# Kernel optimization log

Hardware: AMD Instinct MI355X
Metric: run time of the kernel (lower is better)

Reference implementation:

```python
import jax, jax.numpy as jnp
import numpy as np

N_NODES = 20000


def _gcn_conv(x, edge_index, W, b):
    """PyG GCNConv: add self-loops, symmetric normalization, x @ W, scatter-add, + bias."""
    n = x.shape[0]
    loops = jnp.arange(n, dtype=edge_index.dtype)
    src = jnp.concatenate([edge_index[0], loops])  # [E+N]
    dst = jnp.concatenate([edge_index[1], loops])  # [E+N]
    # degree of target nodes (edge weight 1), self-loops guarantee deg >= 1
    deg = jax.ops.segment_sum(jnp.ones_like(dst, dtype=x.dtype), dst, num_segments=n)
    dinv = jax.lax.rsqrt(deg)
    norm = dinv[src] * dinv[dst]  # [E+N]
    h = x @ W  # [n, out] dense GEMM before aggregation (standard GCNConv ordering)
    msg = h[src] * norm[:, None]  # gather + scale over edges
    out = jax.ops.segment_sum(msg, dst, num_segments=n)  # scatter-add to targets
    return out + b


def setup_inputs() -> dict:
    key = jax.random.key(0)
    k = jax.random.split(key, 6)
    in_f, h_f, n_cls = 512, 512, 256
    x = jax.random.normal(k[0], (N_NODES, in_f), dtype=jnp.float32)
    edge_index = jax.random.randint(k[1], (2, 160000), 0, N_NODES, dtype=jnp.int64)
    W1 = jax.random.normal(k[2], (in_f, h_f), dtype=jnp.float32) * (1.0 / np.sqrt(in_f))
    b1 = jnp.zeros((h_f,), dtype=jnp.float32)
    W2 = jax.random.normal(k[3], (h_f, n_cls), dtype=jnp.float32) * (1.0 / np.sqrt(h_f))
    b2 = jnp.zeros((n_cls,), dtype=jnp.float32)
    return {"x": x, "edge_index": edge_index, "W1": W1, "b1": b1, "W2": W2, "b2": b2}


def reference(x, edge_index, W1, b1, W2, b2):
    h = jax.nn.relu(_gcn_conv(x, edge_index, W1, b1))
    h = jax.nn.relu(_gcn_conv(h, edge_index, W2, b2))
    # F.dropout in eval mode is identity; reference is deterministic eval-mode forward
    return h
```

## Files before the change

kernel.cpp:

```cpp
#include <hip/hip_runtime.h>


typedef __bf16 bf16x8 __attribute__((ext_vector_type(8)));
typedef float floatx4 __attribute__((ext_vector_type(4)));
typedef unsigned short ushort_t;
typedef unsigned int uint_t;

#define MAXD 32
#define CAP 40

__device__ inline ushort_t f2bf(float f) {
    unsigned u = __builtin_bit_cast(unsigned, f);
    unsigned r = (u + 0x7FFFu + ((u >> 16) & 1u)) >> 16;
    return (ushort_t)r;
}
__device__ inline float bf_lo(uint_t u) { return __builtin_bit_cast(float, u << 16); }
__device__ inline float bf_hi(uint_t u) { return __builtin_bit_cast(float, u & 0xFFFF0000u); }
__device__ inline uint_t pk2(float lo, float hi) {
    return (uint_t)f2bf(lo) | ((uint_t)f2bf(hi) << 16);
}

__device__ inline void transpose_tile(const float* __restrict__ in,
                                      ushort_t* __restrict__ out,
                                      int K, int N, int k0, int n0,
                                      ushort_t (*tile)[33]) {
    int tx = threadIdx.x & 31, ty = threadIdx.x >> 5;
    for (int r = ty; r < 32; r += 8)
        tile[r][tx] = f2bf(in[(size_t)(k0 + r) * N + n0 + tx]);
    __syncthreads();
    for (int r = ty; r < 32; r += 8)
        out[(size_t)(n0 + r) * K + k0 + tx] = tile[tx][r];
}

__global__ __launch_bounds__(256) void prep_fused(
    const int* __restrict__ src, const int* __restrict__ dst,
    int* __restrict__ deg, int* __restrict__ col_ell,
    int* __restrict__ ovf_cnt, int* __restrict__ ovf, int e, int nb_e,
    const float* __restrict__ x, ushort_t* __restrict__ xb, long xcount, int nb_conv,
    const float* __restrict__ W1, ushort_t* __restrict__ w1t,
    const float* __restrict__ W2, ushort_t* __restrict__ w2t) {
    __shared__ ushort_t tile[32][33];
    int b = blockIdx.x;
    if (b < nb_e) {
        int i = b * 256 + threadIdx.x;
        if (i < e) {
            int s = src[i], d = dst[i];
            int slot = atomicAdd(&deg[d], 1);
            if (slot < MAXD) {
                col_ell[d * MAXD + slot] = s;
            } else {
                int k = atomicAdd(ovf_cnt, 1);
                ovf[2 * k] = d;
                ovf[2 * k + 1] = s;
            }
        }
        return;
    }
    b -= nb_e;
    if (b < nb_conv) {
        long i = ((long)b * 256 + threadIdx.x) * 4;
        if (i < xcount) {
            float4 v = *(const float4*)(x + i);
            ushort4 o = make_ushort4(f2bf(v.x), f2bf(v.y), f2bf(v.z), f2bf(v.w));
            *(ushort4*)(xb + i) = o;
        }
        return;
    }
    b -= nb_conv;
    if (b < 256) {
        transpose_tile(W1, w1t, 512, 512, (b >> 4) * 32, (b & 15) * 32, tile);
        return;
    }
    b -= 256;
    transpose_tile(W2, w2t, 512, 256, (b >> 3) * 32, (b & 7) * 32, tile);
}

__global__ __launch_bounds__(256) void gemm_mfma(
    const ushort_t* __restrict__ A, const ushort_t* __restrict__ BT,
    ushort_t* __restrict__ C,
    int M, int N, int K, int nbx, int gemm_blocks,
    const int* __restrict__ deg, float* __restrict__ dinv_out, int n) {
    __shared__ __align__(16) ushort_t As[8192];
    __shared__ __align__(16) ushort_t Bs[8192];

    if ((int)blockIdx.x >= gemm_blocks) {
        int i = ((int)blockIdx.x - gemm_blocks) * 256 + threadIdx.x;
        if (i < n) dinv_out[i] = 1.0f / sqrtf((float)(deg[i] + 1));
        return;
    }

    const int bx = (int)blockIdx.x % nbx, by = (int)blockIdx.x / nbx;
    const int tid = threadIdx.x;
    const int w = tid >> 6, lane = tid & 63;
    const int q = lane >> 4, ml = lane & 15;
    const int wm = (w >> 1) * 64, wn = (w & 1) * 64;
    const int row0 = by * 128, col0 = bx * 128;

    const int rr = lane >> 3;
    const int gsw = (lane & 7) ^ (rr & 7);
    const ushort_t* ga[4];
    const ushort_t* gb[4];
    ushort_t* la[4];
    ushort_t* lb[4];
#pragma unroll
    for (int rp = 0; rp < 4; rp++) {
        int r = rp * 32 + w * 8 + rr;
        int gra = min(row0 + r, M - 1);
        ga[rp] = A + (size_t)gra * K + gsw * 8;
        gb[rp] = BT + (size_t)(col0 + r) * K + gsw * 8;
        la[rp] = As + rp * 2048 + w * 512;
        lb[rp] = Bs + rp * 2048 + w * 512;
    }

    const int sel = ml & 7;
    int aoff[2][4], boff[2][4];
#pragma unroll
    for (int st = 0; st < 2; st++)
#pragma unroll
        for (int i = 0; i < 4; i++) {
            int g = q + st * 4;
            aoff[st][i] = (wm + i * 16 + ml) * 64 + ((g ^ sel) << 3);
            boff[st][i] = (wn + i * 16 + ml) * 64 + ((g ^ sel) << 3);
        }

    floatx4 acc[4][4];
#pragma unroll
    for (int i = 0; i < 4; i++)
#pragma unroll
        for (int j = 0; j < 4; j++) acc[i][j] = (floatx4)0.0f;

    for (int kt = 0; kt < K; kt += 64) {
#pragma unroll
        for (int rp = 0; rp < 4; rp++) {
            __builtin_amdgcn_global_load_lds(
                (const __attribute__((address_space(1))) unsigned*)ga[rp],
                (__attribute__((address_space(3))) unsigned*)la[rp], 16, 0, 0);
            __builtin_amdgcn_global_load_lds(
                (const __attribute__((address_space(1))) unsigned*)gb[rp],
                (__attribute__((address_space(3))) unsigned*)lb[rp], 16, 0, 0);
            ga[rp] += 64; gb[rp] += 64;
        }
        __syncthreads();
#pragma unroll
        for (int st = 0; st < 2; st++) {
            bf16x8 af[4], bfr[4];
#pragma unroll
            for (int i = 0; i < 4; i++) {
                af[i] = *(const bf16x8*)(As + aoff[st][i]);
                bfr[i] = *(const bf16x8*)(Bs + boff[st][i]);
            }
#pragma unroll
            for (int i = 0; i < 4; i++)
#pragma unroll
                for (int j = 0; j < 4; j++)
                    acc[i][j] = __builtin_amdgcn_mfma_f32_16x16x32_bf16(
                        af[i], bfr[j], acc[i][j], 0, 0, 0);
        }
        __syncthreads();
    }

#pragma unroll
    for (int i = 0; i < 4; i++) {
        int rbase = row0 + wm + i * 16 + q * 4;
#pragma unroll
        for (int j = 0; j < 4; j++) {
            int gc = col0 + wn + j * 16 + ml;
#pragma unroll
            for (int r = 0; r < 4; r++) {
                int gr = rbase + r;
                if (gr < M) C[(size_t)gr * N + gc] = f2bf(acc[i][j][r]);
            }
        }
    }
}

__global__ __launch_bounds__(256, 2) void agg1gemm2(
    const ushort_t* __restrict__ g,
    const ushort_t* __restrict__ BT,
    const int* __restrict__ deg, const int* __restrict__ col_ell,
    const int* __restrict__ ovf_cnt, const int* __restrict__ ovf,
    const float* __restrict__ dinv, const float* __restrict__ b1,
    ushort_t* __restrict__ g2, int M) {
    __shared__ __align__(16) ushort_t As[16 * 512];
    __shared__ __align__(16) ushort_t Bs[256 * 64];
    __shared__ int2  adj_s[16][CAP];
    __shared__ float b1_s[512];
    __shared__ int   cnt_s[16];

    const int tid = threadIdx.x;
    const int w = tid >> 6, lane = tid & 63;
    const int q = lane >> 4, ml = lane & 15;
    const int wn = w * 64;
    const int row0 = (int)blockIdx.x * 16;

    for (int i = tid; i < 512; i += 256) b1_s[i] = b1[i];
    {
        int r = tid >> 4, jj = tid & 15;
        int rg = min(row0 + r, M - 1);
        int cnt = min(deg[rg], MAXD);
        const int* cm = col_ell + (size_t)rg * MAXD;
#pragma unroll
        for (int pass = 0; pass < 3; pass++) {
            int j = jj + pass * 16;
            if (j >= CAP) break;
            int2 a;
            if (j == 0) {
                a.x = rg;
                a.y = __builtin_bit_cast(int, dinv[rg]);
                cnt_s[r] = cnt + 1;
            } else {
                bool vld = (j - 1) < cnt;
                int c = vld ? cm[j - 1] : rg;
                a.x = c;
                a.y = vld ? __builtin_bit_cast(int, dinv[c]) : 0;
            }
            adj_s[r][j] = a;
        }
    }
    const int nov = *ovf_cnt;
    __syncthreads();

    const int rr = lane >> 3;
    const int gsw = (lane & 7) ^ (rr & 7);
    const ushort_t* gb[8];
    ushort_t* lb[8];
#pragma unroll
    for (int rp = 0; rp < 8; rp++) {
        gb[rp] = BT + (size_t)(rp * 32 + w * 8 + rr) * 512 + gsw * 8;
        lb[rp] = Bs + (rp * 32 + w * 8) * 64;
    }
#pragma unroll
    for (int rp = 0; rp < 8; rp++) {
        __builtin_amdgcn_global_load_lds(
            (const __attribute__((address_space(1))) unsigned*)gb[rp],
            (__attribute__((address_space(3))) unsigned*)lb[rp], 16, 0, 0);
        gb[rp] += 64;
    }

    const int c = lane;
    const ushort_t* gc_ = g + c * 8;
    float4 bv0 = *(const float4*)(b1_s + c * 8);
    float4 bv1 = *(const float4*)(b1_s + c * 8 + 4);

#pragma unroll
    for (int p = 0; p < 4; p++) {
        const int rP = p * 4 + w;
        const int cntR = cnt_s[rP];
        const float pdr = __builtin_bit_cast(float, adj_s[rP][0].y);
        const int selfR = adj_s[rP][0].x;

        float a0 = 0.f, a1 = 0.f, a2 = 0.f, a3 = 0.f;
        float a4 = 0.f, a5 = 0.f, a6 = 0.f, a7 = 0.f;

        for (int e0 = 0; e0 < cntR; e0 += 8) {
            int2 cp[8];
#pragma unroll
            for (int j = 0; j < 8; j++) cp[j] = adj_s[rP][e0 + j];
            uint4 u[8];
#pragma unroll
            for (int j = 0; j < 8; j++)
                u[j] = *(const uint4*)(gc_ + (size_t)cp[j].x * 512);
#pragma unroll
            for (int j = 0; j < 8; j++) {
                float ps = __builtin_bit_cast(float, cp[j].y);
                a0 = fmaf(ps, bf_lo(u[j].x), a0);
                a1 = fmaf(ps, bf_hi(u[j].x), a1);
                a2 = fmaf(ps, bf_lo(u[j].y), a2);
                a3 = fmaf(ps, bf_hi(u[j].y), a3);
                a4 = fmaf(ps, bf_lo(u[j].z), a4);
                a5 = fmaf(ps, bf_hi(u[j].z), a5);
                a6 = fmaf(ps, bf_lo(u[j].w), a6);
                a7 = fmaf(ps, bf_hi(u[j].w), a7);
            }
        }
        for (int k2 = 0; k2 < nov; k2++) {
            if (ovf[2 * k2] == selfR) {
                int sI = ovf[2 * k2 + 1];
                float ps = dinv[sI];
                uint4 u = *(const uint4*)(gc_ + (size_t)sI * 512);
                a0 = fmaf(ps, bf_lo(u.x), a0);
                a1 = fmaf(ps, bf_hi(u.x), a1);
                a2 = fmaf(ps, bf_lo(u.y), a2);
                a3 = fmaf(ps, bf_hi(u.y), a3);
                a4 = fmaf(ps, bf_lo(u.z), a4);
                a5 = fmaf(ps, bf_hi(u.z), a5);
                a6 = fmaf(ps, bf_lo(u.w), a6);
                a7 = fmaf(ps, bf_hi(u.w), a7);
            }
        }
        float h0 = fmaxf(fmaf(pdr, a0, bv0.x), 0.0f);
        float h1 = fmaxf(fmaf(pdr, a1, bv0.y), 0.0f);
        float h2 = fmaxf(fmaf(pdr, a2, bv0.z), 0.0f);
        float h3 = fmaxf(fmaf(pdr, a3, bv0.w), 0.0f);
        float h4 = fmaxf(fmaf(pdr, a4, bv1.x), 0.0f);
        float h5 = fmaxf(fmaf(pdr, a5, bv1.y), 0.0f);
        float h6 = fmaxf(fmaf(pdr, a6, bv1.z), 0.0f);
        float h7 = fmaxf(fmaf(pdr, a7, bv1.w), 0.0f);
        uint4 U;
        U.x = pk2(h0, h1);
        U.y = pk2(h2, h3);
        U.z = pk2(h4, h5);
        U.w = pk2(h6, h7);
        int pos = (c & ~7) | ((c & 7) ^ (rP & 7));
        *(uint4*)(As + rP * 512 + pos * 8) = U;
    }

    const int sel = ml & 7;
    int aoffb[2], boff[2][4];
#pragma unroll
    for (int st = 0; st < 2; st++) {
        aoffb[st] = ml * 512 + (((st * 4 + q) ^ sel) << 3);
#pragma unroll
        for (int i = 0; i < 4; i++)
            boff[st][i] = (wn + i * 16 + ml) * 64 + (((q + st * 4) ^ sel) << 3);
    }
    floatx4 accm[4];
#pragma unroll
    for (int j = 0; j < 4; j++) accm[j] = (floatx4)0.0f;

    for (int kt = 0; kt < 8; kt++) {
        __syncthreads();
#pragma unroll
        for (int st = 0; st < 2; st++) {
            bf16x8 af = *(const bf16x8*)(As + aoffb[st] + kt * 64);
#pragma unroll
            for (int j = 0; j < 4; j++) {
                bf16x8 bfr = *(const bf16x8*)(Bs + boff[st][j]);
                accm[j] = __builtin_amdgcn_mfma_f32_16x16x32_bf16(af, bfr,
                                                                  accm[j], 0, 0, 0);
            }
        }
        __syncthreads();
        if (kt < 7) {
#pragma unroll
            for (int rp = 0; rp < 8; rp++) {
                __builtin_amdgcn_global_load_lds(
                    (const __attribute__((address_space(1))) unsigned*)gb[rp],
                    (__attribute__((address_space(3))) unsigned*)lb[rp], 16, 0, 0);
                gb[rp] += 64;
            }
        }
    }

#pragma unroll
    for (int j = 0; j < 4; j++) {
        int gcx = wn + j * 16 + ml;
#pragma unroll
        for (int rg = 0; rg < 4; rg++) {
            int lrow = q * 4 + rg;
            int grow = row0 + lrow;
            if (grow < M) {
                float pd = __builtin_bit_cast(float, adj_s[lrow][0].y);
                g2[(size_t)grow * 256 + gcx] = f2bf(pd * accm[j][rg]);
            }
        }
    }
}

__global__ __launch_bounds__(64) void aggregate2(const uint2* __restrict__ g,
                                                 const int* __restrict__ deg,
                                                 const int* __restrict__ col_ell,
                                                 const int* __restrict__ ovf_cnt,
                                                 const int* __restrict__ ovf,
                                                 const float* __restrict__ dinv,
                                                 const float* __restrict__ bias,
                                                 float* __restrict__ out) {
    const int d = blockIdx.x, t = threadIdx.x;
    const int cnt = min(deg[d], MAXD);
    const float pd = dinv[d];
    const size_t base = (size_t)d * 64 + t;
    const int* cm = col_ell + (size_t)d * MAXD;

    int cv = 0;
    float wv = 0.0f;
    if (t < MAXD && t < cnt) {
        cv = cm[t];
        wv = 1.0f;
    }
    float4 b = *(const float4*)(bias + t * 4);

    uint2 us = g[base];
    float a0 = bf_lo(us.x), a1 = bf_hi(us.x);
    float a2 = bf_lo(us.y), a3 = bf_hi(us.y);

    for (int e0 = 0; e0 < cnt; e0 += 8) {
        uint2 u[8];
        float ws[8];
#pragma unroll
        for (int j = 0; j < 8; j++) {
            int s = __shfl(cv, e0 + j);
            ws[j] = __shfl(wv, e0 + j);
            u[j] = g[(size_t)s * 64 + t];
        }
#pragma unroll
        for (int j = 0; j < 8; j++) {
            a0 = fmaf(ws[j], bf_lo(u[j].x), a0);
            a1 = fmaf(ws[j], bf_hi(u[j].x), a1);
            a2 = fmaf(ws[j], bf_lo(u[j].y), a2);
            a3 = fmaf(ws[j], bf_hi(u[j].y), a3);
        }
    }
    int nov = *ovf_cnt;
    for (int k = 0; k < nov; k++) {
        if (ovf[2 * k] == d) {
            uint2 u = g[(size_t)ovf[2 * k + 1] * 64 + t];
            a0 += bf_lo(u.x); a1 += bf_hi(u.x);
            a2 += bf_lo(u.y); a3 += bf_hi(u.y);
        }
    }
    float4 o;
    o.x = fmaxf(fmaf(pd, a0, b.x), 0.0f);
    o.y = fmaxf(fmaf(pd, a1, b.y), 0.0f);
    o.z = fmaxf(fmaf(pd, a2, b.z), 0.0f);
    o.w = fmaxf(fmaf(pd, a3, b.w), 0.0f);
    *(float4*)(out + (size_t)d * 256 + t * 4) = o;
}

extern "C" void kernel_launch(void* const* d_in, const int* in_sizes, int n_in,
                              void* d_out, int out_size, void* d_ws, size_t ws_size,
                              hipStream_t stream) {
    const float* x  = (const float*)d_in[0];
    const int*   ei = (const int*)d_in[1];
    const float* W1 = (const float*)d_in[2];
    const float* b1 = (const float*)d_in[3];
    const float* W2 = (const float*)d_in[4];
    const float* b2 = (const float*)d_in[5];
    float* out = (float*)d_out;

    const int FIN = 512, FH = 512, FOUT = 256;
    const int n = in_sizes[0] / FIN;
    const int e = in_sizes[1] / 2;
    const int* src = ei;
    const int* dst = ei + e;

    auto align_up = [](size_t v) { return (v + 255) & ~(size_t)255; };
    char* w = (char*)d_ws;
    int*      deg     = (int*)w;
    int*      ovf_cnt = deg + n;
    w += align_up((size_t)(n + 1) * 4);
    float*    dinv    = (float*)w;    w += align_up((size_t)n * 4);
    int*      col_ell = (int*)w;      w += align_up((size_t)n * MAXD * 4);
    int*      ovf     = (int*)w;      w += align_up((size_t)2048 * 4);
    ushort_t* xb      = (ushort_t*)w; w += align_up((size_t)n * FIN * 2);
    ushort_t* w1t     = (ushort_t*)w; w += align_up((size_t)FH * FIN * 2);
    ushort_t* w2t     = (ushort_t*)w; w += align_up((size_t)FOUT * FH * 2);
    ushort_t* g       = (ushort_t*)w; w += align_up((size_t)n * FH * 2);
    ushort_t* g2      = (ushort_t*)w; w += align_up((size_t)n * FOUT * 2);

    const int nb_n = (n + 255) / 256;
    const int nb_e = (e + 255) / 256;
    const long xcount = (long)n * FIN;
    const int nb_conv = (int)((xcount / 4 + 255) / 256);

    hipMemsetAsync(deg, 0, (size_t)(n + 1) * 4, stream);

    prep_fused<<<nb_e + nb_conv + 256 + 128, 256, 0, stream>>>(
        src, dst, deg, col_ell, ovf_cnt, ovf, e, nb_e,
        x, xb, xcount, nb_conv, W1, w1t, W2, w2t);

    {
        const int mb = (n + 127) / 128;
        int gemm_blocks = (FH / 128) * mb;
        gemm_mfma<<<gemm_blocks + nb_n, 256, 0, stream>>>(
            xb, w1t, g, n, FH, FIN, FH / 128, gemm_blocks, deg, dinv, n);
    }
    agg1gemm2<<<(n + 15) / 16, 256, 0, stream>>>(
        g, w2t, deg, col_ell, ovf_cnt, ovf, dinv, b1, g2, n);

    aggregate2<<<n, 64, 0, stream>>>((const uint2*)g2, deg, col_ell, ovf_cnt,
                                     ovf, dinv, b2, out);

    (void)ws_size; (void)n_in; (void)out_size;
}
```

Measured before the change: 188.1 us.

## Halve B-tile LDS in agg1gemm2 by splitting N into two chunks for occupancy

```diff
diff --git a/kernel.cpp b/kernel.cpp
--- a/kernel.cpp
+++ b/kernel.cpp
@@ -174,7 +174,7 @@
     }
 }
 
-__global__ __launch_bounds__(256, 2) void agg1gemm2(
+__global__ __launch_bounds__(256, 4) void agg1gemm2(
     const ushort_t* __restrict__ g,
     const ushort_t* __restrict__ BT,
     const int* __restrict__ deg, const int* __restrict__ col_ell,
@@ -182,7 +182,7 @@
     const float* __restrict__ dinv, const float* __restrict__ b1,
     ushort_t* __restrict__ g2, int M) {
     __shared__ __align__(16) ushort_t As[16 * 512];
-    __shared__ __align__(16) ushort_t Bs[256 * 64];
+    __shared__ __align__(16) ushort_t Bs[128 * 64];
     __shared__ int2  adj_s[16][CAP];
     __shared__ float b1_s[512];
     __shared__ int   cnt_s[16];
@@ -190,7 +190,6 @@
     const int tid = threadIdx.x;
     const int w = tid >> 6, lane = tid & 63;
     const int q = lane >> 4, ml = lane & 15;
-    const int wn = w * 64;
     const int row0 = (int)blockIdx.x * 16;
 
     for (int i = tid; i < 512; i += 256) b1_s[i] = b1[i];
@@ -222,19 +221,17 @@
 
     const int rr = lane >> 3;
     const int gsw = (lane & 7) ^ (rr & 7);
-    const ushort_t* gb[8];
-    ushort_t* lb[8];
-#pragma unroll
-    for (int rp = 0; rp < 8; rp++) {
-        gb[rp] = BT + (size_t)(rp * 32 + w * 8 + rr) * 512 + gsw * 8;
+    ushort_t* lb[4];
+#pragma unroll
+    for (int rp = 0; rp < 4; rp++)
         lb[rp] = Bs + (rp * 32 + w * 8) * 64;
-    }
-#pragma unroll
-    for (int rp = 0; rp < 8; rp++) {
+
+#pragma unroll
+    for (int rp = 0; rp < 4; rp++) {
+        const ushort_t* src = BT + (size_t)(rp * 32 + w * 8 + rr) * 512 + gsw * 8;
         __builtin_amdgcn_global_load_lds(
-            (const __attribute__((address_space(1))) unsigned*)gb[rp],
+            (const __attribute__((address_space(1))) unsigned*)src,
             (__attribute__((address_space(3))) unsigned*)lb[rp], 16, 0, 0);
-        gb[rp] += 64;
     }
 
     const int c = lane;
@@ -306,52 +303,57 @@
     }
 
     const int sel = ml & 7;
-    int aoffb[2], boff[2][4];
+    int aoffb[2], boff[2][2];
 #pragma unroll
     for (int st = 0; st < 2; st++) {
         aoffb[st] = ml * 512 + (((st * 4 + q) ^ sel) << 3);
 #pragma unroll
-        for (int i = 0; i < 4; i++)
-            boff[st][i] = (wn + i * 16 + ml) * 64 + (((q + st * 4) ^ sel) << 3);
+        for (int j = 0; j < 2; j++)
+            boff[st][j] = (w * 32 + j * 16 + ml) * 64 + (((q + st * 4) ^ sel) << 3);
     }
     floatx4 accm[4];
 #pragma unroll
     for (int j = 0; j < 4; j++) accm[j] = (floatx4)0.0f;
 
-    for (int kt = 0; kt < 8; kt++) {
+    for (int s = 0; s < 16; s++) {
+        const int ch = s >> 3, kt = s & 7;
         __syncthreads();
 #pragma unroll
         for (int st = 0; st < 2; st++) {
             bf16x8 af = *(const bf16x8*)(As + aoffb[st] + kt * 64);
 #pragma unroll
-            for (int j = 0; j < 4; j++) {
+            for (int j = 0; j < 2; j++) {
                 bf16x8 bfr = *(const bf16x8*)(Bs + boff[st][j]);
-                accm[j] = __builtin_amdgcn_mfma_f32_16x16x32_bf16(af, bfr,
-                                                                  accm[j], 0, 0, 0);
+                accm[ch * 2 + j] = __builtin_amdgcn_mfma_f32_16x16x32_bf16(
+                    af, bfr, accm[ch * 2 + j], 0, 0, 0);
             }
         }
         __syncthreads();
-        if (kt < 7) {
-#pragma unroll
-            for (int rp = 0; rp < 8; rp++) {
+        if (s < 15) {
+            const int ns = s + 1, nch = ns >> 3, nkt = ns & 7;
+#pragma unroll
+            for (int rp = 0; rp < 4; rp++) {
+                const ushort_t* src = BT +
+                    (size_t)(nch * 128 + rp * 32 + w * 8 + rr) * 512 +
+                    gsw * 8 + nkt * 64;
                 __builtin_amdgcn_global_load_lds(
-                    (const __attribute__((address_space(1))) unsigned*)gb[rp],
+                    (const __attribute__((address_space(1))) unsigned*)src,
                     (__attribute__((address_space(3))) unsigned*)lb[rp], 16, 0, 0);
-                gb[rp] += 64;
-            }
-        }
-    }
-
-#pragma unroll
-    for (int j = 0; j < 4; j++) {
-        int gcx = wn + j * 16 + ml;
+            }
+        }
+    }
+
+#pragma unroll
+    for (int idx = 0; idx < 4; idx++) {
+        int ch = idx >> 1, j = idx & 1;
+        int gcx = ch * 128 + w * 32 + j * 16 + ml;
 #pragma unroll
         for (int rg = 0; rg < 4; rg++) {
             int lrow = q * 4 + rg;
             int grow = row0 + lrow;
             if (grow < M) {
                 float pd = __builtin_bit_cast(float, adj_s[lrow][0].y);
-                g2[(size_t)grow * 256 + gcx] = f2bf(pd * accm[j][rg]);
+                g2[(size_t)grow * 256 + gcx] = f2bf(pd * accm[idx][rg]);
             }
         }
     }
```

New measurement: 184.1 us. 1.02x faster.
